# Optimization experiments

Hardware: AMD Instinct MI355X
Metric: run time of the kernel (lower is better)

Reference implementation:

```python
import jax, jax.numpy as jnp
import numpy as np
import math

PS = 8  # patch size (hard-coded in module)
DEPTH = 6
LAMBDA_INIT = 0.8 - 0.6 * math.exp(-0.3 * DEPTH)

# torch_dct norm=None DCT-II matrix: y_k = 2 * sum_n x_n cos(pi*(2n+1)k/(2N))
_n = np.arange(PS)
_C = 2.0 * np.cos(np.pi * (2 * _n[None, :] + 1) * _n[:, None] / (2 * PS))  # [k, n]
_Ci = np.linalg.inv(_C)
DCT_M = jnp.asarray(_C, jnp.float32)
IDCT_M = jnp.asarray(_Ci, jnp.float32)


def dct2(x):  # 2D DCT over last two dims (torch_dct.dct_2d, norm=None)
    return jnp.einsum('...mn,am,bn->...ab', x, DCT_M, DCT_M)


def idct2(x):  # exact inverse (torch_dct.idct_2d, norm=None)
    return jnp.einsum('...ab,ma,nb->...mn', x, IDCT_M, IDCT_M)


def conv1x1(x, w):  # w: [O, I]
    return jnp.einsum('oi,bihw->bohw', w, x)


def dw3(x, w):  # depthwise 3x3, stride 1, pad 1; w: [C, 1, 3, 3]
    return jax.lax.conv_general_dilated(
        x, w, window_strides=(1, 1), padding='SAME',
        dimension_numbers=('NCHW', 'OIHW', 'NCHW'),
        feature_group_count=x.shape[1])


def prelu(t, a):
    return jnp.where(t >= 0, t, a * t)


def setup_inputs() -> dict:
    key = jax.random.key(0)
    ks = jax.random.split(key, 20)
    b, c, H, W = 2, 64, 384, 384
    w = lambda k, shape: jax.random.normal(k, shape, jnp.float32) * 0.05
    heads = c // 16
    return {
        'x': jax.random.normal(ks[0], (b, c, H, W), jnp.float32),
        'nir': jax.random.normal(ks[1], (b, c, H, W), jnp.float32),
        'w_hidden': w(ks[2], (c, c)),
        'w_hidden_nir': w(ks[3], (2 * c, c)),
        'w_dw': w(ks[4], (c, 1, 3, 3)),
        'w_dw_nir': w(ks[5], (2 * c, 1, 3, 3)),
        'temperature': jnp.ones((heads, 1, 1), jnp.float32),
        'w_proj_mid': w(ks[6], (c, c)),
        'w_proj_out': w(ks[7], (c, c)),
        'w_p1a': w(ks[8], (c, 1, 3, 3)),
        'a_p1': jnp.asarray(0.25, jnp.float32),
        'w_p1b': w(ks[9], (c, 1, 3, 3)),
        'w_p2a': w(ks[10], (c, 1, 3, 3)),
        'a_p2': jnp.asarray(0.25, jnp.float32),
        'w_p2b': w(ks[11], (c, 1, 3, 3)),
        'lq1': jax.random.normal(ks[12], (c,), jnp.float32) * 0.1,
        'lk1': jax.random.normal(ks[13], (c,), jnp.float32) * 0.1,
        'lq2': jax.random.normal(ks[14], (c,), jnp.float32) * 0.1,
        'lk2': jax.random.normal(ks[15], (c,), jnp.float32) * 0.1,
    }


def reference(x, nir, w_hidden, w_hidden_nir, w_dw, w_dw_nir, temperature,
              w_proj_mid, w_proj_out, w_p1a, a_p1, w_p1b, w_p2a, a_p2, w_p2b,
              lq1, lk1, lq2, lk2):
    b, c, H, W = x.shape
    heads = c // 16
    hh, ww = H // PS, W // PS

    hidden = conv1x1(x, w_hidden)
    nir_hidden = conv1x1(nir, w_hidden_nir)
    q = dw3(hidden, w_dw)
    kv = dw3(nir_hidden, w_dw_nir)
    k, v = kv[:, :c], kv[:, c:]

    # b c (hh p1) (ww p2) -> b c hh ww p1 p2
    patch = lambda t: t.reshape(b, c, hh, PS, ww, PS).transpose(0, 1, 2, 4, 3, 5)
    q_fft = dct2(patch(q))
    k_fft = dct2(patch(k))
    out1 = q_fft * k_fft

    L = hh * ww * PS * PS
    hf = lambda t: t.reshape(b, heads, c // heads, L)  # b head c L
    q_fft, k_fft, out1f = hf(q_fft), hf(k_fft), hf(out1)

    qn = q_fft / jnp.maximum(jnp.linalg.norm(q_fft, axis=-1, keepdims=True), 1e-12)
    kn = k_fft / jnp.maximum(jnp.linalg.norm(k_fft, axis=-1, keepdims=True), 1e-12)

    attn = jax.nn.softmax(jnp.einsum('bhcl,bhdl->bhcd', qn, kn) * temperature, axis=-1)
    o = jnp.einsum('bhcd,bhdl->bhcl', attn, out1f)

    o = o.reshape(b, c, hh, ww, PS, PS)
    o = idct2(o)
    o = o.transpose(0, 1, 2, 4, 3, 5).reshape(b, c, H, W)
    out = conv1x1(o, w_proj_mid)

    lam1 = jnp.exp(jnp.sum(lq1 * lk1))
    lam2 = jnp.exp(jnp.sum(lq2 * lk2))
    lam = lam1 - lam2 + LAMBDA_INIT

    pool = lambda t, wa, a, wb: dw3(prelu(dw3(t, wa), a), wb)
    output = pool(q * out, w_p1a, a_p1, w_p1b) + pool(v - lam * (v * out), w_p2a, a_p2, w_p2b)
    return conv1x1(output, w_proj_out)
```

## Files before the change

### kernel.cpp

```cpp
#include <hip/hip_runtime.h>
#include <cmath>

#ifndef M_PI
#define M_PI 3.14159265358979323846
#endif

#define NB      2
#define N_PIX   147456
#define L_LEN   147456
#define TENS_SZ ((long)NB * 64 * N_PIX)

#define OFF_C    0
#define OFF_CI   64
#define OFF_LAM  128
#define OFF_GRAM 256
#define OFF_QQ   2304
#define OFF_KK   2432
#define OFF_ATTN 2560

#define TW 128
#define TH 16
#define LW 136
#define LH 18
#define PLH 20

__global__ __launch_bounds__(64) void init_k(const float* __restrict__ lq1, const float* __restrict__ lk1,
                                             const float* __restrict__ lq2, const float* __restrict__ lk2,
                                             float* __restrict__ sm) {
  int t = threadIdx.x;
  int a = t >> 3, m = t & 7;
  double cv = 2.0 * cos(M_PI * (double)((2 * m + 1) * a) / 16.0);
  sm[OFF_C + a * 8 + m] = (float)cv;
  sm[OFF_CI + m * 8 + a] = (float)(cv / ((a == 0) ? 32.0 : 16.0));
  float p1 = lq1[t] * lk1[t];
  float p2 = lq2[t] * lk2[t];
  #pragma unroll
  for (int off = 32; off; off >>= 1) {
    p1 += __shfl_xor(p1, off, 64);
    p2 += __shfl_xor(p2, off, 64);
  }
  if (t == 0) sm[OFF_LAM] = expf(p1) - expf(p2) + 0.70082066706704813f;
  for (int i = t; i < 2304; i += 64) sm[OFF_GRAM + i] = 0.f;
}

__global__ void diag_k(float* out, float v) { out[0] = v; }

__global__ __launch_bounds__(256) void conv1x1_k(const float* __restrict__ in, const float* __restrict__ w,
                                                 float* __restrict__ out) {
  __shared__ float ws[4096];
  int t = threadIdx.x;
  for (int j = t; j < 1024; j += 256)
    *reinterpret_cast<float4*>(ws + j * 4) = *reinterpret_cast<const float4*>(w + j * 4);
  __syncthreads();

  long gp = (long)blockIdx.x * 256;
  int bb = (int)(gp / N_PIX);
  int p0 = (int)(gp - (long)bb * N_PIX);
  int lane = t & 63;
  int co0 = (t >> 6) * 16;

  const float* ip = in + (long)bb * 64 * N_PIX + p0 + lane * 4;
  const float* wp = ws + co0 * 64;

  float acc[16][4];
  #pragma unroll
  for (int j = 0; j < 16; j++)
    #pragma unroll
    for (int p = 0; p < 4; p++) acc[j][p] = 0.f;

  for (int c4 = 0; c4 < 16; c4++) {
    float4 x0 = *reinterpret_cast<const float4*>(ip + (long)(c4 * 4 + 0) * N_PIX);
    float4 x1 = *reinterpret_cast<const float4*>(ip + (long)(c4 * 4 + 1) * N_PIX);
    float4 x2 = *reinterpret_cast<const float4*>(ip + (long)(c4 * 4 + 2) * N_PIX);
    float4 x3 = *reinterpret_cast<const float4*>(ip + (long)(c4 * 4 + 3) * N_PIX);
    #pragma unroll
    for (int j = 0; j < 16; j++) {
      float4 w4 = *reinterpret_cast<const float4*>(wp + j * 64 + c4 * 4);
      acc[j][0] = fmaf(w4.x, x0.x, acc[j][0]);
      acc[j][0] = fmaf(w4.y, x1.x, acc[j][0]);
      acc[j][0] = fmaf(w4.z, x2.x, acc[j][0]);
      acc[j][0] = fmaf(w4.w, x3.x, acc[j][0]);
      acc[j][1] = fmaf(w4.x, x0.y, acc[j][1]);
      acc[j][1] = fmaf(w4.y, x1.y, acc[j][1]);
      acc[j][1] = fmaf(w4.z, x2.y, acc[j][1]);
      acc[j][1] = fmaf(w4.w, x3.y, acc[j][1]);
      acc[j][2] = fmaf(w4.x, x0.z, acc[j][2]);
      acc[j][2] = fmaf(w4.y, x1.z, acc[j][2]);
      acc[j][2] = fmaf(w4.z, x2.z, acc[j][2]);
      acc[j][2] = fmaf(w4.w, x3.z, acc[j][2]);
      acc[j][3] = fmaf(w4.x, x0.w, acc[j][3]);
      acc[j][3] = fmaf(w4.y, x1.w, acc[j][3]);
      acc[j][3] = fmaf(w4.z, x2.w, acc[j][3]);
      acc[j][3] = fmaf(w4.w, x3.w, acc[j][3]);
    }
  }

  float* op = out + (long)bb * 64 * N_PIX + p0 + lane * 4;
  #pragma unroll
  for (int j = 0; j < 16; j++)
    *reinterpret_cast<float4*>(op + (long)(co0 + j) * N_PIX) =
        make_float4(acc[j][0], acc[j][1], acc[j][2], acc[j][3]);
}

__device__ __forceinline__ float4 load_g4(const float* __restrict__ p, int gy, int gx) {
  if ((unsigned)gy >= 384u) return make_float4(0.f, 0.f, 0.f, 0.f);
  if (gx >= 0 && gx + 3 < 384) return *reinterpret_cast<const float4*>(p + gy * 384 + gx);
  float e[4];
  #pragma unroll
  for (int i = 0; i < 4; i++) {
    int xx = gx + i;
    e[i] = ((unsigned)xx < 384u) ? p[gy * 384 + xx] : 0.f;
  }
  return make_float4(e[0], e[1], e[2], e[3]);
}

__global__ __launch_bounds__(256) void dw3t_k(const float* __restrict__ in, const float* __restrict__ w,
                                              float* __restrict__ out) {
  __shared__ float sT[LH * LW];
  int plane = blockIdx.z;
  int ch = plane & 63;
  int x0 = blockIdx.x * TW, y0 = blockIdx.y * TH;
  const float* ip = in + (long)plane * N_PIX;
  int t = threadIdx.x;
  for (int j = t; j < LH * 34; j += 256) {
    int row = j / 34, c4 = j - row * 34;
    *reinterpret_cast<float4*>(sT + row * LW + c4 * 4) = load_g4(ip, y0 - 1 + row, x0 - 4 + c4 * 4);
  }
  __syncthreads();
  const float* wp = w + ch * 9;
  float w00 = wp[0], w01 = wp[1], w02 = wp[2];
  float w10 = wp[3], w11 = wp[4], w12 = wp[5];
  float w20 = wp[6], w21 = wp[7], w22 = wp[8];
  int col = t & 127, rg = t >> 7;
  int lc = col + 4;
  int r0 = rg * 8;
  float a0 = sT[r0 * LW + lc - 1],       a1 = sT[r0 * LW + lc],       a2 = sT[r0 * LW + lc + 1];
  float b0 = sT[(r0 + 1) * LW + lc - 1], b1 = sT[(r0 + 1) * LW + lc], b2 = sT[(r0 + 1) * LW + lc + 1];
  float* op = out + (long)plane * N_PIX + (long)(y0 + rg * 8) * 384 + x0 + col;
  #pragma unroll
  for (int i = 0; i < 8; i++) {
    int lr = r0 + i + 2;
    float c0 = sT[lr * LW + lc - 1], c1 = sT[lr * LW + lc], c2 = sT[lr * LW + lc + 1];
    float s = w00 * a0;
    s = fmaf(w01, a1, s); s = fmaf(w02, a2, s);
    s = fmaf(w10, b0, s); s = fmaf(w11, b1, s); s = fmaf(w12, b2, s);
    s = fmaf(w20, c0, s); s = fmaf(w21, c1, s); s = fmaf(w22, c2, s);
    op[i * 384] = s;
    a0 = b0; a1 = b1; a2 = b2;
    b0 = c0; b1 = c1; b2 = c2;
  }
}

__device__ __forceinline__ void stencil_col9(const float* __restrict__ sb, int ci, int rs0,
                                             float w00, float w01, float w02,
                                             float w10, float w11, float w12,
                                             float w20, float w21, float w22,
                                             float alpha, bool xok, int y0,
                                             float* __restrict__ r) {
  float a0 = sb[rs0 * LW + ci - 1],       a1 = sb[rs0 * LW + ci],       a2 = sb[rs0 * LW + ci + 1];
  float b0 = sb[(rs0 + 1) * LW + ci - 1], b1 = sb[(rs0 + 1) * LW + ci], b2 = sb[(rs0 + 1) * LW + ci + 1];
  #pragma unroll
  for (int ii = 0; ii < 9; ii++) {
    int rs2 = rs0 + ii + 2;
    float c0 = sb[rs2 * LW + ci - 1], c1 = sb[rs2 * LW + ci], c2 = sb[rs2 * LW + ci + 1];
    float s = w00 * a0;
    s = fmaf(w01, a1, s); s = fmaf(w02, a2, s);
    s = fmaf(w10, b0, s); s = fmaf(w11, b1, s); s = fmaf(w12, b2, s);
    s = fmaf(w20, c0, s); s = fmaf(w21, c1, s); s = fmaf(w22, c2, s);
    s = (s >= 0.f) ? s : alpha * s;
    int gy = y0 - 1 + rs0 + ii;
    r[ii] = (xok && (unsigned)gy < 384u) ? s : 0.f;
    a0 = b0; a1 = b1; a2 = b2;
    b0 = c0; b1 = c1; b2 = c2;
  }
}

__global__ __launch_bounds__(256) void pool_k(const float* __restrict__ q, const float* __restrict__ om,
                                              const float* __restrict__ v,
                                              const float* __restrict__ w1a, const float* __restrict__ a1p,
                                              const float* __restrict__ w1b,
                                              const float* __restrict__ w2a, const float* __restrict__ a2p,
                                              const float* __restrict__ w2b,
                                              const float* __restrict__ sm,
                                              float* __restrict__ outp) {
  __shared__ float s1[PLH * LW], s2[PLH * LW];
  int plane = blockIdx.z;
  int ch = plane & 63;
  int x0 = blockIdx.x * TW, y0 = blockIdx.y * TH;
  const float* qp = q  + (long)plane * N_PIX;
  const float* op = om + (long)plane * N_PIX;
  const float* vp = v  + (long)plane * N_PIX;
  float lam = sm[OFF_LAM];
  int t = threadIdx.x;
  for (int j = t; j < PLH * 34; j += 256) {
    int row = j / 34, c4 = j - row * 34;
    int gy = y0 - 2 + row, gx = x0 - 4 + c4 * 4;
    float4 qv = load_g4(qp, gy, gx);
    float4 ov = load_g4(op, gy, gx);
    float4 vv = load_g4(vp, gy, gx);
    *reinterpret_cast<float4*>(s1 + row * LW + c4 * 4) =
        make_float4(qv.x * ov.x, qv.y * ov.y, qv.z * ov.z, qv.w * ov.w);
    *reinterpret_cast<float4*>(s2 + row * LW + c4 * 4) =
        make_float4(vv.x - lam * vv.x * ov.x, vv.y - lam * vv.y * ov.y,
                    vv.z - lam * vv.z * ov.z, vv.w - lam * vv.w * ov.w);
  }
  __syncthreads();

  int ct = t & 127, rg = t >> 7;
  int rs0 = rg * 9;
  int ci0 = 3 + ct;
  int ci1 = 131 + ct;
  bool xok0 = (unsigned)(x0 - 4 + ci0) < 384u;
  bool xok1 = (unsigned)(x0 - 4 + ci1) < 384u;

  {
    const float* wp1 = w1a + ch * 9;
    float w00 = wp1[0], w01 = wp1[1], w02 = wp1[2], w10 = wp1[3], w11 = wp1[4],
          w12 = wp1[5], w20 = wp1[6], w21 = wp1[7], w22 = wp1[8];
    float alpha = a1p[0];
    float rm[9], re[9];
    stencil_col9(s1, ci0, rs0, w00, w01, w02, w10, w11, w12, w20, w21, w22, alpha, xok0, y0, rm);
    if (ct < 2)
      stencil_col9(s1, ci1, rs0, w00, w01, w02, w10, w11, w12, w20, w21, w22, alpha, xok1, y0, re);
    __syncthreads();
    #pragma unroll
    for (int ii = 0; ii < 9; ii++) s1[(rs0 + ii + 1) * LW + ci0] = rm[ii];
    if (ct < 2) {
      #pragma unroll
      for (int ii = 0; ii < 9; ii++) s1[(rs0 + ii + 1) * LW + ci1] = re[ii];
    }
  }
  {
    const float* wp2 = w2a + ch * 9;
    float w00 = wp2[0], w01 = wp2[1], w02 = wp2[2], w10 = wp2[3], w11 = wp2[4],
          w12 = wp2[5], w20 = wp2[6], w21 = wp2[7], w22 = wp2[8];
    float alpha = a2p[0];
    float rm[9], re[9];
    stencil_col9(s2, ci0, rs0, w00, w01, w02, w10, w11, w12, w20, w21, w22, alpha, xok0, y0, rm);
    if (ct < 2)
      stencil_col9(s2, ci1, rs0, w00, w01, w02, w10, w11, w12, w20, w21, w22, alpha, xok1, y0, re);
    __syncthreads();
    #pragma unroll
    for (int ii = 0; ii < 9; ii++) s2[(rs0 + ii + 1) * LW + ci0] = rm[ii];
    if (ct < 2) {
      #pragma unroll
      for (int ii = 0; ii < 9; ii++) s2[(rs0 + ii + 1) * LW + ci1] = re[ii];
    }
  }
  __syncthreads();
  {
    const float* wp1 = w1b + ch * 9;
    const float* wp2 = w2b + ch * 9;
    float p00 = wp1[0], p01 = wp1[1], p02 = wp1[2], p10 = wp1[3], p11 = wp1[4], p12 = wp1[5], p20 = wp1[6], p21 = wp1[7], p22 = wp1[8];
    float q00 = wp2[0], q01 = wp2[1], q02 = wp2[2], q10 = wp2[3], q11 = wp2[4], q12 = wp2[5], q20 = wp2[6], q21 = wp2[7], q22 = wp2[8];
    int col = t & 127, rg2 = t >> 7;
    int lc = col + 4;
    int rb = rg2 * 8 + 1;
    float xa0 = s1[rb * LW + lc - 1],       xa1 = s1[rb * LW + lc],       xa2 = s1[rb * LW + lc + 1];
    float xb0 = s1[(rb + 1) * LW + lc - 1], xb1 = s1[(rb + 1) * LW + lc], xb2 = s1[(rb + 1) * LW + lc + 1];
    float ya0 = s2[rb * LW + lc - 1],       ya1 = s2[rb * LW + lc],       ya2 = s2[rb * LW + lc + 1];
    float yb0 = s2[(rb + 1) * LW + lc - 1], yb1 = s2[(rb + 1) * LW + lc], yb2 = s2[(rb + 1) * LW + lc + 1];
    float* wo = outp + (long)plane * N_PIX + (long)(y0 + rg2 * 8) * 384 + x0 + col;
    #pragma unroll
    for (int i = 0; i < 8; i++) {
      int lr = rb + i + 2;
      float xc0 = s1[lr * LW + lc - 1], xc1 = s1[lr * LW + lc], xc2 = s1[lr * LW + lc + 1];
      float yc0 = s2[lr * LW + lc - 1], yc1 = s2[lr * LW + lc], yc2 = s2[lr * LW + lc + 1];
      float s = p00 * xa0;
      s = fmaf(p01, xa1, s); s = fmaf(p02, xa2, s);
      s = fmaf(p10, xb0, s); s = fmaf(p11, xb1, s); s = fmaf(p12, xb2, s);
      s = fmaf(p20, xc0, s); s = fmaf(p21, xc1, s); s = fmaf(p22, xc2, s);
      s = fmaf(q00, ya0, s); s = fmaf(q01, ya1, s); s = fmaf(q02, ya2, s);
      s = fmaf(q10, yb0, s); s = fmaf(q11, yb1, s); s = fmaf(q12, yb2, s);
      s = fmaf(q20, yc0, s); s = fmaf(q21, yc1, s); s = fmaf(q22, yc2, s);
      wo[i * 384] = s;
      xa0 = xb0; xa1 = xb1; xa2 = xb2; xb0 = xc0; xb1 = xc1; xb2 = xc2;
      ya0 = yb0; ya1 = yb1; ya2 = yb2; yb0 = yc0; yb1 = yc1; yb2 = yc2;
    }
  }
}

__global__ __launch_bounds__(256) void dct_k(const float* __restrict__ in,
                                             const float* __restrict__ sm, float* __restrict__ outf) {
  __shared__ float Cm[64];
  if (threadIdx.x < 64) Cm[threadIdx.x] = sm[OFF_C + threadIdx.x];
  __syncthreads();
  int pid = blockIdx.x * 256 + threadIdx.x;
  int wx = pid % 48;
  int t1 = pid / 48;
  int hy = t1 % 48; t1 /= 48;
  int ch = t1 & 63;
  int bb = t1 >> 6;
  const float* ip = in + (long)(bb * 64 + ch) * N_PIX + (hy * 8) * 384 + wx * 8;
  float X[8][8];
  #pragma unroll
  for (int r = 0; r < 8; r++) {
    float4 v0 = *reinterpret_cast<const float4*>(ip + r * 384);
    float4 v1 = *reinterpret_cast<const float4*>(ip + r * 384 + 4);
    X[r][0] = v0.x; X[r][1] = v0.y; X[r][2] = v0.z; X[r][3] = v0.w;
    X[r][4] = v1.x; X[r][5] = v1.y; X[r][6] = v1.z; X[r][7] = v1.w;
  }
  float T[8][8];
  #pragma unroll
  for (int a = 0; a < 8; a++)
    #pragma unroll
    for (int n = 0; n < 8; n++) {
      float s = 0.f;
      #pragma unroll
      for (int m = 0; m < 8; m++) s = fmaf(Cm[a * 8 + m], X[m][n], s);
      T[a][n] = s;
    }
  #pragma unroll
  for (int a = 0; a < 8; a++)
    #pragma unroll
    for (int b8 = 0; b8 < 8; b8++) {
      float s = 0.f;
      #pragma unroll
      for (int n = 0; n < 8; n++) s = fmaf(Cm[b8 * 8 + n], T[a][n], s);
      X[a][b8] = s;
    }
  float* op = outf + (long)(bb * 64 + ch) * L_LEN + (long)(hy * 48 + wx) * 64;
  float4* o4 = reinterpret_cast<float4*>(op);
  #pragma unroll
  for (int a = 0; a < 8; a++) {
    o4[a * 2]     = make_float4(X[a][0], X[a][1], X[a][2], X[a][3]);
    o4[a * 2 + 1] = make_float4(X[a][4], X[a][5], X[a][6], X[a][7]);
  }
}

#define GS_P 132
__global__ __launch_bounds__(256) void gram_k(const float* __restrict__ qf, const float* __restrict__ kf,
                                              float* __restrict__ sm) {
  __shared__ float qs[16 * GS_P], ks[16 * GS_P];
  int t = threadIdx.x;
  int bh = blockIdx.y;
  int bb = bh >> 2, h = bh & 3;
  const float* qbase = qf + ((long)bb * 64 + h * 16) * L_LEN;
  const float* kbase = kf + ((long)bb * 64 + h * 16) * L_LEN;
  int c = t >> 4, d = t & 15;
  long l0 = (long)blockIdx.x * 2048;
  float g = 0.f, nq = 0.f, nk = 0.f;
  for (int chunk = 0; chunk < 16; chunk++) {
    long lc = l0 + chunk * 128;
    __syncthreads();
    for (int j = t; j < 512; j += 256) {
      int row = j >> 5, c4 = j & 31;
      *reinterpret_cast<float4*>(qs + row * GS_P + c4 * 4) =
          *reinterpret_cast<const float4*>(qbase + (long)row * L_LEN + lc + c4 * 4);
      *reinterpret_cast<float4*>(ks + row * GS_P + c4 * 4) =
          *reinterpret_cast<const float4*>(kbase + (long)row * L_LEN + lc + c4 * 4);
    }
    __syncthreads();
    #pragma unroll
    for (int i = 0; i < 128; i += 4) {
      float4 a = *reinterpret_cast<const float4*>(qs + c * GS_P + i);
      float4 b = *reinterpret_cast<const float4*>(ks + d * GS_P + i);
      g  = fmaf(a.x, b.x, g);  g  = fmaf(a.y, b.y, g);  g  = fmaf(a.z, b.z, g);  g  = fmaf(a.w, b.w, g);
      nq = fmaf(a.x, a.x, nq); nq = fmaf(a.y, a.y, nq); nq = fmaf(a.z, a.z, nq); nq = fmaf(a.w, a.w, nq);
      nk = fmaf(b.x, b.x, nk); nk = fmaf(b.y, b.y, nk); nk = fmaf(b.z, b.z, nk); nk = fmaf(b.w, b.w, nk);
    }
  }
  atomicAdd(&sm[OFF_GRAM + bh * 256 + c * 16 + d], g);
  if (d == 0) atomicAdd(&sm[OFF_QQ + bh * 16 + c], nq);
  if (c == 0) atomicAdd(&sm[OFF_KK + bh * 16 + d], nk);
}

__global__ __launch_bounds__(256) void attn_k(const float* __restrict__ temp, float* __restrict__ sm) {
  int bh = blockIdx.x;
  int h = bh & 3;
  int t = threadIdx.x;
  int c = t >> 4, d = t & 15;
  float qn = fmaxf(sqrtf(sm[OFF_QQ + bh * 16 + c]), 1e-12f);
  float kn = fmaxf(sqrtf(sm[OFF_KK + bh * 16 + d]), 1e-12f);
  float v = sm[OFF_GRAM + bh * 256 + t] / (qn * kn) * temp[h];
  float mx = v;
  #pragma unroll
  for (int o = 8; o; o >>= 1) mx = fmaxf(mx, __shfl_xor(mx, o, 16));
  float e = expf(v - mx);
  float s = e;
  #pragma unroll
  for (int o = 8; o; o >>= 1) s += __shfl_xor(s, o, 16);
  sm[OFF_ATTN + bh * 256 + t] = e / s;
}

#define CB_P 273
__global__ __launch_bounds__(256) void comb_idct_k(const float* __restrict__ qf, const float* __restrict__ kf,
                                                   const float* __restrict__ sm, float* __restrict__ out) {
  __shared__ float A[256];
  __shared__ float Ci[64];
  __shared__ float sb[16 * CB_P];
  int bh = blockIdx.y;
  int t = threadIdx.x;
  A[t] = sm[OFF_ATTN + bh * 256 + t];
  if (t < 64) Ci[t] = sm[OFF_CI + t];
  __syncthreads();
  int bb = bh >> 2, h = bh & 3;
  long l = (long)blockIdx.x * 256 + t;
  const float* qp = qf + ((long)bb * 64 + h * 16) * L_LEN + l;
  const float* kp = kf + ((long)bb * 64 + h * 16) * L_LEN + l;
  float p[16];
  #pragma unroll
  for (int d = 0; d < 16; d++) p[d] = qp[(long)d * L_LEN] * kp[(long)d * L_LEN];
  int pl_w = t >> 6, i_w = t & 63;
  #pragma unroll
  for (int c = 0; c < 16; c++) {
    float s = 0.f;
    #pragma unroll
    for (int d = 0; d < 16; d++) s = fmaf(A[c * 16 + d], p[d], s);
    sb[c * CB_P + pl_w * 68 + i_w] = s;
  }
  __syncthreads();
  int j = t & 3, c = (t >> 2) & 15, pl = t >> 6;
  const float* fb = sb + c * CB_P + pl * 68;
  float F[8][8];
  #pragma unroll
  for (int a = 0; a < 8; a++)
    #pragma unroll
    for (int b8 = 0; b8 < 8; b8++) F[a][b8] = fb[a * 8 + b8];
  int patch = blockIdx.x * 4 + pl;
  int hy = patch / 48, wx = patch - hy * 48;
  float* op = out + ((long)bb * 64 + h * 16 + c) * N_PIX + (long)(hy * 8) * 384 + wx * 8;
  #pragma unroll
  for (int mm = 0; mm < 2; mm++) {
    int m = 2 * j + mm;
    float T[8];
    #pragma unroll
    for (int b8 = 0; b8 < 8; b8++) {
      float s = 0.f;
      #pragma unroll
      for (int a = 0; a < 8; a++) s = fmaf(Ci[m * 8 + a], F[a][b8], s);
      T[b8] = s;
    }
    float o[8];
    #pragma unroll
    for (int n = 0; n < 8; n++) {
      float s = 0.f;
      #pragma unroll
      for (int b8 = 0; b8 < 8; b8++) s = fmaf(Ci[n * 8 + b8], T[b8], s);
      o[n] = s;
    }
    *reinterpret_cast<float4*>(op + m * 384)     = make_float4(o[0], o[1], o[2], o[3]);
    *reinterpret_cast<float4*>(op + m * 384 + 4) = make_float4(o[4], o[5], o[6], o[7]);
  }
}

__global__ __launch_bounds__(256) void combine_k(float* __restrict__ qf, const float* __restrict__ kf,
                                                 const float* __restrict__ sm) {
  __shared__ float A[256];
  int bh = blockIdx.y;
  A[threadIdx.x] = sm[OFF_ATTN + bh * 256 + threadIdx.x];
  __syncthreads();
  int bb = bh >> 2, h = bh & 3;
  long l = (long)blockIdx.x * 256 + threadIdx.x;
  float* qp = qf + ((long)bb * 64 + h * 16) * L_LEN + l;
  const float* kp = kf + ((long)bb * 64 + h * 16) * L_LEN + l;
  float p[16];
  #pragma unroll
  for (int d = 0; d < 16; d++) p[d] = qp[(long)d * L_LEN] * kp[(long)d * L_LEN];
  #pragma unroll
  for (int c = 0; c < 16; c++) {
    float s = 0.f;
    #pragma unroll
    for (int d = 0; d < 16; d++) s = fmaf(A[c * 16 + d], p[d], s);
    qp[(long)c * L_LEN] = s;
  }
}

__global__ __launch_bounds__(256) void idct_k(const float* __restrict__ inf, const float* __restrict__ sm,
                                              float* __restrict__ out) {
  __shared__ float Ci[64];
  if (threadIdx.x < 64) Ci[threadIdx.x] = sm[OFF_CI + threadIdx.x];
  __syncthreads();
  int pid = blockIdx.x * 256 + threadIdx.x;
  int wx = pid % 48;
  int t1 = pid / 48;
  int hy = t1 % 48; t1 /= 48;
  int ch = t1 & 63;
  int bb = t1 >> 6;
  const float4* i4 = reinterpret_cast<const float4*>(inf + (long)(bb * 64 + ch) * L_LEN + (long)(hy * 48 + wx) * 64);
  float F[8][8];
  #pragma unroll
  for (int a = 0; a < 8; a++) {
    float4 v0 = i4[a * 2], v1 = i4[a * 2 + 1];
    F[a][0] = v0.x; F[a][1] = v0.y; F[a][2] = v0.z; F[a][3] = v0.w;
    F[a][4] = v1.x; F[a][5] = v1.y; F[a][6] = v1.z; F[a][7] = v1.w;
  }
  float T[8][8];
  #pragma unroll
  for (int m = 0; m < 8; m++)
    #pragma unroll
    for (int b8 = 0; b8 < 8; b8++) {
      float s = 0.f;
      #pragma unroll
      for (int a = 0; a < 8; a++) s = fmaf(Ci[m * 8 + a], F[a][b8], s);
      T[m][b8] = s;
    }
  #pragma unroll
  for (int m = 0; m < 8; m++)
    #pragma unroll
    for (int n = 0; n < 8; n++) {
      float s = 0.f;
      #pragma unroll
      for (int b8 = 0; b8 < 8; b8++) s = fmaf(Ci[n * 8 + b8], T[m][b8], s);
      F[m][n] = s;
    }
  float* op = out + (long)(bb * 64 + ch) * N_PIX + (hy * 8) * 384 + wx * 8;
  #pragma unroll
  for (int m = 0; m < 8; m++) {
    *reinterpret_cast<float4*>(op + m * 384)     = make_float4(F[m][0], F[m][1], F[m][2], F[m][3]);
    *reinterpret_cast<float4*>(op + m * 384 + 4) = make_float4(F[m][4], F[m][5], F[m][6], F[m][7]);
  }
}

extern "C" void kernel_launch(void* const* d_in, const int* in_sizes, int n_in,
                              void* d_out, int out_size, void* d_ws, size_t ws_size,
                              hipStream_t stream) {
  const float* x            = (const float*)d_in[0];
  const float* nir          = (const float*)d_in[1];
  const float* w_hidden     = (const float*)d_in[2];
  const float* w_hidden_nir = (const float*)d_in[3];
  const float* w_dw         = (const float*)d_in[4];
  const float* w_dw_nir     = (const float*)d_in[5];
  const float* temperature  = (const float*)d_in[6];
  const float* w_proj_mid   = (const float*)d_in[7];
  const float* w_proj_out   = (const float*)d_in[8];
  const float* w_p1a        = (const float*)d_in[9];
  const float* a_p1         = (const float*)d_in[10];
  const float* w_p1b        = (const float*)d_in[11];
  const float* w_p2a        = (const float*)d_in[12];
  const float* a_p2         = (const float*)d_in[13];
  const float* w_p2b        = (const float*)d_in[14];
  const float* lq1          = (const float*)d_in[15];
  const float* lk1          = (const float*)d_in[16];
  const float* lq2          = (const float*)d_in[17];
  const float* lk2          = (const float*)d_in[18];

  float* OUT = (float*)d_out;
  float* W0 = (float*)d_ws;
  float* W1 = W0 + TENS_SZ;
  float* W2 = W1 + TENS_SZ;
  float* SM = W2 + TENS_SZ;
  float* W3 = SM + 8192;

  size_t needed3 = (size_t)3 * TENS_SZ * sizeof(float) + 32768;
  size_t needed4 = ((size_t)4 * TENS_SZ + 8192) * sizeof(float);
  if (ws_size < needed3) {
    diag_k<<<1, 1, 0, stream>>>(OUT, 1000.0f + (float)(ws_size >> 20));
    return;
  }
  bool big = ws_size >= needed4;

  dim3 blk256(256);
  dim3 gridST(3, 24, NB * 64);

  init_k<<<1, 64, 0, stream>>>(lq1, lk1, lq2, lk2, SM);
  conv1x1_k<<<1152, blk256, 0, stream>>>(x, w_hidden, W0);
  dw3t_k<<<gridST, blk256, 0, stream>>>(W0, w_dw, OUT);
  conv1x1_k<<<1152, blk256, 0, stream>>>(nir, w_hidden_nir, W0);
  dw3t_k<<<gridST, blk256, 0, stream>>>(W0, w_dw_nir, W1);
  conv1x1_k<<<1152, blk256, 0, stream>>>(nir, w_hidden_nir + 64 * 64, W0);
  dw3t_k<<<gridST, blk256, 0, stream>>>(W0, w_dw_nir + 64 * 9, W2);
  dct_k<<<1152, blk256, 0, stream>>>(W1, SM, W0);
  dct_k<<<1152, blk256, 0, stream>>>(OUT, SM, W1);
  gram_k<<<dim3(72, 8), blk256, 0, stream>>>(W1, W0, SM);
  attn_k<<<8, blk256, 0, stream>>>(temperature, SM);

  float* o_spatial;
  if (big) {
    comb_idct_k<<<dim3(576, 8), blk256, 0, stream>>>(W1, W0, SM, W3);
    o_spatial = W3;
  } else {
    combine_k<<<dim3(576, 8), blk256, 0, stream>>>(W1, W0, SM);
    idct_k<<<1152, blk256, 0, stream>>>(W1, SM, W0);
    o_spatial = W0;
  }
  conv1x1_k<<<1152, blk256, 0, stream>>>(o_spatial, w_proj_mid, W1);
  pool_k<<<gridST, blk256, 0, stream>>>(OUT, W1, W2, w_p1a, a_p1, w_p1b, w_p2a, a_p2, w_p2b, SM, W0);
  conv1x1_k<<<1152, blk256, 0, stream>>>(W0, w_proj_out, OUT);
}
```

Baseline: 773.1 us.

## Fuse depthwise conv with DCT and merge the two nir 1x1 convs

```diff
diff --git a/kernel.cpp b/kernel.cpp
--- a/kernel.cpp
+++ b/kernel.cpp
@@ -102,6 +102,62 @@
         make_float4(acc[j][0], acc[j][1], acc[j][2], acc[j][3]);
 }
 
+__global__ __launch_bounds__(256) void conv1x1_nir2_k(const float* __restrict__ in, const float* __restrict__ w,
+                                                      float* __restrict__ outk, float* __restrict__ outv) {
+  __shared__ float ws[4096];
+  int t = threadIdx.x;
+  long gp = (long)blockIdx.x * 256;
+  int bb = (int)(gp / N_PIX);
+  int p0 = (int)(gp - (long)bb * N_PIX);
+  int lane = t & 63;
+  int co0 = (t >> 6) * 16;
+  const float* ip = in + (long)bb * 64 * N_PIX + p0 + lane * 4;
+
+  for (int half = 0; half < 2; half++) {
+    __syncthreads();
+    for (int j = t; j < 1024; j += 256)
+      *reinterpret_cast<float4*>(ws + j * 4) = *reinterpret_cast<const float4*>(w + half * 4096 + j * 4);
+    __syncthreads();
+    const float* wp = ws + co0 * 64;
+    float acc[16][4];
+    #pragma unroll
+    for (int j = 0; j < 16; j++)
+      #pragma unroll
+      for (int p = 0; p < 4; p++) acc[j][p] = 0.f;
+    for (int c4 = 0; c4 < 16; c4++) {
+      float4 x0 = *reinterpret_cast<const float4*>(ip + (long)(c4 * 4 + 0) * N_PIX);
+      float4 x1 = *reinterpret_cast<const float4*>(ip + (long)(c4 * 4 + 1) * N_PIX);
+      float4 x2 = *reinterpret_cast<const float4*>(ip + (long)(c4 * 4 + 2) * N_PIX);
+      float4 x3 = *reinterpret_cast<const float4*>(ip + (long)(c4 * 4 + 3) * N_PIX);
+      #pragma unroll
+      for (int j = 0; j < 16; j++) {
+        float4 w4 = *reinterpret_cast<const float4*>(wp + j * 64 + c4 * 4);
+        acc[j][0] = fmaf(w4.x, x0.x, acc[j][0]);
+        acc[j][0] = fmaf(w4.y, x1.x, acc[j][0]);
+        acc[j][0] = fmaf(w4.z, x2.x, acc[j][0]);
+        acc[j][0] = fmaf(w4.w, x3.x, acc[j][0]);
+        acc[j][1] = fmaf(w4.x, x0.y, acc[j][1]);
+        acc[j][1] = fmaf(w4.y, x1.y, acc[j][1]);
+        acc[j][1] = fmaf(w4.z, x2.y, acc[j][1]);
+        acc[j][1] = fmaf(w4.w, x3.y, acc[j][1]);
+        acc[j][2] = fmaf(w4.x, x0.z, acc[j][2]);
+        acc[j][2] = fmaf(w4.y, x1.z, acc[j][2]);
+        acc[j][2] = fmaf(w4.z, x2.z, acc[j][2]);
+        acc[j][2] = fmaf(w4.w, x3.z, acc[j][2]);
+        acc[j][3] = fmaf(w4.x, x0.w, acc[j][3]);
+        acc[j][3] = fmaf(w4.y, x1.w, acc[j][3]);
+        acc[j][3] = fmaf(w4.z, x2.w, acc[j][3]);
+        acc[j][3] = fmaf(w4.w, x3.w, acc[j][3]);
+      }
+    }
+    float* op = (half ? outv : outk) + (long)bb * 64 * N_PIX + p0 + lane * 4;
+    #pragma unroll
+    for (int j = 0; j < 16; j++)
+      *reinterpret_cast<float4*>(op + (long)(co0 + j) * N_PIX) =
+          make_float4(acc[j][0], acc[j][1], acc[j][2], acc[j][3]);
+  }
+}
+
 __device__ __forceinline__ float4 load_g4(const float* __restrict__ p, int gy, int gx) {
   if ((unsigned)gy >= 384u) return make_float4(0.f, 0.f, 0.f, 0.f);
   if (gx >= 0 && gx + 3 < 384) return *reinterpret_cast<const float4*>(p + gy * 384 + gx);
@@ -149,6 +205,80 @@
     a0 = b0; a1 = b1; a2 = b2;
     b0 = c0; b1 = c1; b2 = c2;
   }
+}
+
+__global__ __launch_bounds__(256) void dw3dct_k(const float* __restrict__ in, const float* __restrict__ w,
+                                                const float* __restrict__ sm,
+                                                float* __restrict__ outf, float* __restrict__ outs) {
+  __shared__ float sT[LH * LW];
+  __shared__ float Cm[64];
+  int t = threadIdx.x;
+  if (t < 64) Cm[t] = sm[OFF_C + t];
+  int plane = blockIdx.z;
+  int ch = plane & 63;
+  int x0 = blockIdx.x * TW, y0 = blockIdx.y * TH;
+  const float* ip = in + (long)plane * N_PIX;
+  for (int j = t; j < LH * 34; j += 256) {
+    int row = j / 34, c4 = j - row * 34;
+    *reinterpret_cast<float4*>(sT + row * LW + c4 * 4) = load_g4(ip, y0 - 1 + row, x0 - 4 + c4 * 4);
+  }
+  __syncthreads();
+  const float* wp = w + ch * 9;
+  float w00 = wp[0], w01 = wp[1], w02 = wp[2];
+  float w10 = wp[3], w11 = wp[4], w12 = wp[5];
+  float w20 = wp[6], w21 = wp[7], w22 = wp[8];
+  int col = t & 127, rg = t >> 7;
+  int lc = col + 4;
+  int r0 = rg * 8;
+  float r[8];
+  {
+    float a0 = sT[r0 * LW + lc - 1],       a1 = sT[r0 * LW + lc],       a2 = sT[r0 * LW + lc + 1];
+    float b0 = sT[(r0 + 1) * LW + lc - 1], b1 = sT[(r0 + 1) * LW + lc], b2 = sT[(r0 + 1) * LW + lc + 1];
+    #pragma unroll
+    for (int i = 0; i < 8; i++) {
+      int lr = r0 + i + 2;
+      float c0 = sT[lr * LW + lc - 1], c1 = sT[lr * LW + lc], c2 = sT[lr * LW + lc + 1];
+      float s = w00 * a0;
+      s = fmaf(w01, a1, s); s = fmaf(w02, a2, s);
+      s = fmaf(w10, b0, s); s = fmaf(w11, b1, s); s = fmaf(w12, b2, s);
+      s = fmaf(w20, c0, s); s = fmaf(w21, c1, s); s = fmaf(w22, c2, s);
+      r[i] = s;
+      a0 = b0; a1 = b1; a2 = b2;
+      b0 = c0; b1 = c1; b2 = c2;
+    }
+  }
+  if (outs) {
+    float* op = outs + (long)plane * N_PIX + (long)(y0 + r0) * 384 + x0 + col;
+    #pragma unroll
+    for (int i = 0; i < 8; i++) op[i * 384] = r[i];
+  }
+  __syncthreads();
+  #pragma unroll
+  for (int i = 0; i < 8; i++) sT[(r0 + i + 1) * LW + lc] = r[i];
+  __syncthreads();
+  int patch = t >> 3, a = t & 7;
+  int prow = patch >> 4, pcol = patch & 15;
+  const float* xb = sT + (prow * 8 + 1) * LW + pcol * 8 + 4;
+  float T[8];
+  #pragma unroll
+  for (int n = 0; n < 8; n++) {
+    float s = 0.f;
+    #pragma unroll
+    for (int m = 0; m < 8; m++) s = fmaf(Cm[a * 8 + m], xb[m * LW + n], s);
+    T[n] = s;
+  }
+  float o[8];
+  #pragma unroll
+  for (int b8 = 0; b8 < 8; b8++) {
+    float s = 0.f;
+    #pragma unroll
+    for (int n = 0; n < 8; n++) s = fmaf(Cm[b8 * 8 + n], T[n], s);
+    o[b8] = s;
+  }
+  int py = (y0 >> 3) + prow, px = (x0 >> 3) + pcol;
+  float* op = outf + (long)plane * L_LEN + (long)(py * 48 + px) * 64 + a * 8;
+  *reinterpret_cast<float4*>(op)     = make_float4(o[0], o[1], o[2], o[3]);
+  *reinterpret_cast<float4*>(op + 4) = make_float4(o[4], o[5], o[6], o[7]);
 }
 
 __device__ __forceinline__ void stencil_col9(const float* __restrict__ sb, int ci, int rs0,
@@ -554,27 +684,34 @@
   dim3 gridST(3, 24, NB * 64);
 
   init_k<<<1, 64, 0, stream>>>(lq1, lk1, lq2, lk2, SM);
-  conv1x1_k<<<1152, blk256, 0, stream>>>(x, w_hidden, W0);
-  dw3t_k<<<gridST, blk256, 0, stream>>>(W0, w_dw, OUT);
-  conv1x1_k<<<1152, blk256, 0, stream>>>(nir, w_hidden_nir, W0);
-  dw3t_k<<<gridST, blk256, 0, stream>>>(W0, w_dw_nir, W1);
-  conv1x1_k<<<1152, blk256, 0, stream>>>(nir, w_hidden_nir + 64 * 64, W0);
-  dw3t_k<<<gridST, blk256, 0, stream>>>(W0, w_dw_nir + 64 * 9, W2);
-  dct_k<<<1152, blk256, 0, stream>>>(W1, SM, W0);
-  dct_k<<<1152, blk256, 0, stream>>>(OUT, SM, W1);
-  gram_k<<<dim3(72, 8), blk256, 0, stream>>>(W1, W0, SM);
-  attn_k<<<8, blk256, 0, stream>>>(temperature, SM);
-
-  float* o_spatial;
+
   if (big) {
-    comb_idct_k<<<dim3(576, 8), blk256, 0, stream>>>(W1, W0, SM, W3);
-    o_spatial = W3;
+    conv1x1_nir2_k<<<1152, blk256, 0, stream>>>(nir, w_hidden_nir, W0, W1);
+    dw3t_k<<<gridST, blk256, 0, stream>>>(W1, w_dw_nir + 64 * 9, W2);
+    dw3dct_k<<<gridST, blk256, 0, stream>>>(W0, w_dw_nir, SM, W1, nullptr);
+    conv1x1_k<<<1152, blk256, 0, stream>>>(x, w_hidden, W0);
+    dw3dct_k<<<gridST, blk256, 0, stream>>>(W0, w_dw, SM, W3, OUT);
+    gram_k<<<dim3(72, 8), blk256, 0, stream>>>(W3, W1, SM);
+    attn_k<<<8, blk256, 0, stream>>>(temperature, SM);
+    comb_idct_k<<<dim3(576, 8), blk256, 0, stream>>>(W3, W1, SM, W0);
+    conv1x1_k<<<1152, blk256, 0, stream>>>(W0, w_proj_mid, W1);
+    pool_k<<<gridST, blk256, 0, stream>>>(OUT, W1, W2, w_p1a, a_p1, w_p1b, w_p2a, a_p2, w_p2b, SM, W3);
+    conv1x1_k<<<1152, blk256, 0, stream>>>(W3, w_proj_out, OUT);
   } else {
+    conv1x1_k<<<1152, blk256, 0, stream>>>(x, w_hidden, W0);
+    dw3t_k<<<gridST, blk256, 0, stream>>>(W0, w_dw, OUT);
+    conv1x1_k<<<1152, blk256, 0, stream>>>(nir, w_hidden_nir, W0);
+    dw3t_k<<<gridST, blk256, 0, stream>>>(W0, w_dw_nir, W1);
+    conv1x1_k<<<1152, blk256, 0, stream>>>(nir, w_hidden_nir + 64 * 64, W0);
+    dw3t_k<<<gridST, blk256, 0, stream>>>(W0, w_dw_nir + 64 * 9, W2);
+    dct_k<<<1152, blk256, 0, stream>>>(W1, SM, W0);
+    dct_k<<<1152, blk256, 0, stream>>>(OUT, SM, W1);
+    gram_k<<<dim3(72, 8), blk256, 0, stream>>>(W1, W0, SM);
+    attn_k<<<8, blk256, 0, stream>>>(temperature, SM);
     combine_k<<<dim3(576, 8), blk256, 0, stream>>>(W1, W0, SM);
     idct_k<<<1152, blk256, 0, stream>>>(W1, SM, W0);
-    o_spatial = W0;
-  }
-  conv1x1_k<<<1152, blk256, 0, stream>>>(o_spatial, w_proj_mid, W1);
-  pool_k<<<gridST, blk256, 0, stream>>>(OUT, W1, W2, w_p1a, a_p1, w_p1b, w_p2a, a_p2, w_p2b, SM, W0);
-  conv1x1_k<<<1152, blk256, 0, stream>>>(W0, w_proj_out, OUT);
-}
+    conv1x1_k<<<1152, blk256, 0, stream>>>(W0, w_proj_mid, W1);
+    pool_k<<<gridST, blk256, 0, stream>>>(OUT, W1, W2, w_p1a, a_p1, w_p1b, w_p2a, a_p2, w_p2b, SM, W0);
+    conv1x1_k<<<1152, blk256, 0, stream>>>(W0, w_proj_out, OUT);
+  }
+}
```

New measurement: 751.2 us. 2.8% less time.
